# Kernel tuning notes

Hardware: AMD Instinct MI355X
Metric: run time of the kernel (lower is better)

## Reference

```python
import jax, jax.numpy as jnp
import numpy as np

B, S, D = 4, 2048, 1024
LAYERS = 2
NLOPS = 4
GAMMA = 0.01          # lindblad_gamma
COND_TH = 100.0       # condition_threshold
EPS = 1e-6


def setup_inputs() -> dict:
    key = jax.random.key(0)
    ks = jax.random.split(key, 9)
    x_real = jax.random.normal(ks[0], (B, S, D), jnp.float32)
    x_imag = jax.random.normal(ks[1], (B, S, D), jnp.float32)
    H_prev = jax.random.uniform(ks[2], (B, D, D), jnp.float32)
    eye = jnp.eye(D, dtype=jnp.float32)
    # base mixing layer (stand-in for ComplexMamba3Layer): near-identity complex linear
    W_real = eye[None, :, :] + 0.02 * jax.random.normal(ks[3], (LAYERS, D, D), jnp.float32)
    W_imag = 0.02 * jax.random.normal(ks[4], (LAYERS, D, D), jnp.float32)
    L_ops = 0.5 * jax.random.normal(ks[5], (LAYERS, NLOPS, D), jnp.float32)
    theta = jax.random.uniform(ks[6], (LAYERS,), jnp.float32, 0.0, 0.5)
    jump_scale = 0.9 * jnp.ones((LAYERS,), jnp.float32)
    kappa_th = 0.1 * jnp.ones((LAYERS,), jnp.float32)   # curvature_threshold per layer
    return dict(x_real=x_real, x_imag=x_imag, H_prev=H_prev,
                W_real=W_real, W_imag=W_imag, L_ops=L_ops,
                theta=theta, jump_scale=jump_scale, kappa_th=kappa_th)


def _v8_forward(x_real, x_imag, H_prev, W_real, W_imag, L_ops, theta, jump_scale, kappa_th):
    psi = jax.lax.complex(x_real, x_imag)  # [B,S,D] complex64
    Hp = H_prev                            # [B,D,D] real (prev Hamiltonian, detached)
    for l in range(LAYERS):
        residual = psi
        # --- base layer: complex linear mix ---
        Wc = jax.lax.complex(W_real[l], W_imag[l])
        out = jnp.einsum('bsd,de->bse', psi, Wc)
        branch_delta = out - residual
        # --- delta-RMS normalize (no_grad -> stop_gradient) ---
        rms = jnp.sqrt(jnp.clip(jnp.mean(branch_delta.real ** 2 + branch_delta.imag ** 2), 1e-12, None))
        rms = jax.lax.stop_gradient(jnp.maximum(rms, 1e-3))
        b = branch_delta / rms
        # --- Lindblad dissipation: diagonal damping gamma * sum_k L_k^2 ---
        damp = GAMMA * jnp.sum(L_ops[l] ** 2, axis=0)  # [D]
        b = b * (1.0 - damp)
        # --- approximate Hamiltonian H = (1/S) sum_s |psi_s><psi_s| (no_grad) ---
        mag = jnp.abs(b)                                # [B,S,D]
        H = jax.lax.stop_gradient(jnp.einsum('bsd,bse->bde', mag, mag) / S)  # [B,D,D]
        # --- hybrid automata: curvature K = ||H - Hp||_F / ||Hp||_F ---
        diff_n = jnp.sqrt(jnp.sum((H - Hp) ** 2, axis=(1, 2)))
        prev_n = jnp.sqrt(jnp.sum(Hp ** 2, axis=(1, 2)))
        K = diff_n / (prev_n + EPS)                     # [B]
        jumped = K > kappa_th[l]
        b = jnp.where(jumped[:, None, None], b * jump_scale[l].astype(jnp.complex64), b)
        Hp = H
        # --- quaternionic escape: diag-based condition estimate, phase rotation ---
        dg = jnp.diagonal(H, axis1=1, axis2=2)          # [B,D]
        cond = jnp.max(dg, axis=1) / (jnp.min(dg, axis=1) + 1e-12)
        escaped = cond > COND_TH
        rot = jnp.exp(1j * theta[l]).astype(jnp.complex64)
        b = jnp.where(escaped[:, None, None], b * rot, b)
        # --- rescale and residual ---
        b = b * rms
        psi = residual + b
    return jnp.stack([psi.real, psi.imag], axis=0)  # [2,B,S,D] float32


def reference(x_real, x_imag, H_prev, W_real, W_imag, L_ops, theta, jump_scale, kappa_th):
    return _v8_forward(x_real, x_imag, H_prev, W_real, W_imag, L_ops, theta, jump_scale, kappa_th)
```

## Files before the change

kernel.cpp:

```cpp
#include <hip/hip_runtime.h>

#define B_ 4
#define S_ 2048
#define D_ 1024
#define M_ (B_*S_)
#define K2_ 2048
#define N2_ 2048
#define NTOT (B_*S_*D_)
#define DD (D_*D_)

typedef __attribute__((ext_vector_type(4))) float f32x4;
typedef __attribute__((ext_vector_type(8))) short short8;
typedef __attribute__((ext_vector_type(4))) unsigned short u16x4;
typedef __attribute__((ext_vector_type(8))) unsigned short u16x8;

static __device__ __forceinline__ unsigned short f2bf(float f) {
    union { float f; unsigned int u; } v; v.f = f;
    unsigned int u = v.u;
    unsigned int r = (u + 0x7fffu + ((u >> 16) & 1u)) >> 16;
    return (unsigned short)r;
}
static __device__ __forceinline__ float bf2f(unsigned short h) {
    union { unsigned int u; float f; } v; v.u = ((unsigned int)h) << 16;
    return v.f;
}


__global__ __launch_bounds__(256, 2) void gemm_main2(const unsigned short* __restrict__ A2,
                                                     const unsigned short* __restrict__ B2T,
                                                     unsigned short* __restrict__ bd2,
                                                     unsigned short* __restrict__ magT,
                                                     float* __restrict__ scal, int l)
{
    __shared__ unsigned short smem[3 * 128 * 64];
    __shared__ float red[4];
    unsigned short* As  = smem;
    unsigned short* Bsr = smem + 8192;
    unsigned short* Bsi = smem + 16384;

    f32x4 accr[4][4], acci[4][4];
#pragma unroll
    for (int i = 0; i < 4; ++i)
#pragma unroll
        for (int j = 0; j < 4; ++j) { accr[i][j] = (f32x4)0.0f; acci[i][j] = (f32x4)0.0f; }

    const int nt = blockIdx.x, mt = blockIdx.y;
    const int tid = threadIdx.x, wave = tid >> 6, lane = tid & 63;
    const int q = lane >> 4, lm = lane & 15;
    const int wm = (wave >> 1) * 64, wn = (wave & 1) * 64;
    const int crow = lane >> 3;
    const int gcol = ((lane & 7) ^ crow) * 8;

    const unsigned short* Ag  = A2  + (long)mt * 128 * K2_;
    const unsigned short* Bgr = B2T + (long)(nt * 128) * K2_;
    const unsigned short* Bgi = B2T + (long)(nt * 128 + 1024) * K2_;

    for (int kt = 0; kt < K2_ / 64; ++kt) {
        const long k0 = (long)kt * 64;
        __syncthreads();
#pragma unroll
        for (int i2 = 0; i2 < 4; ++i2) {
            int c   = i2 * 4 + wave;
            int row = c * 8 + crow;
            long go = (long)row * K2_ + k0 + gcol;
            __builtin_amdgcn_global_load_lds((const __attribute__((address_space(1))) void*)(Ag + go),
                                             (__attribute__((address_space(3))) void*)(As + c * 512), 16, 0, 0);
            __builtin_amdgcn_global_load_lds((const __attribute__((address_space(1))) void*)(Bgr + go),
                                             (__attribute__((address_space(3))) void*)(Bsr + c * 512), 16, 0, 0);
            __builtin_amdgcn_global_load_lds((const __attribute__((address_space(1))) void*)(Bgi + go),
                                             (__attribute__((address_space(3))) void*)(Bsi + c * 512), 16, 0, 0);
        }
        __syncthreads();
#pragma unroll
        for (int kk = 0; kk < 64; kk += 32) {
            short8 a[4], br[4], bi[4];
#pragma unroll
            for (int t = 0; t < 4; ++t) {
                int arow  = wm + t * 16 + lm;
                int aslot = ((kk >> 3) + q) ^ (arow & 7);
                a[t] = *(const short8*)(As + arow * 64 + aslot * 8);
                int brow  = wn + t * 16 + lm;
                int bslot = ((kk >> 3) + q) ^ (brow & 7);
                br[t] = *(const short8*)(Bsr + brow * 64 + bslot * 8);
                bi[t] = *(const short8*)(Bsi + brow * 64 + bslot * 8);
            }
#pragma unroll
            for (int um = 0; um < 4; ++um)
#pragma unroll
                for (int un = 0; un < 4; ++un) {
                    accr[um][un] = __builtin_amdgcn_mfma_f32_16x16x32_bf16(a[um], br[un], accr[um][un], 0, 0, 0);
                    acci[um][un] = __builtin_amdgcn_mfma_f32_16x16x32_bf16(a[um], bi[un], acci[um][un], 0, 0, 0);
                }
        }
    }

    __syncthreads();
    unsigned short* magLds = smem;
    float ss = 0.f;
#pragma unroll
    for (int um = 0; um < 4; ++um) {
#pragma unroll
        for (int un = 0; un < 4; ++un) {
            int colb = wn + un * 16 + lm;
            int coln = nt * 128 + colb;
            u16x4 magv;
#pragma unroll
            for (int i = 0; i < 4; ++i) {
                long rowm = (long)mt * 128 + wm + um * 16 + q * 4 + i;
                float vr = accr[um][un][i];
                float vi = acci[um][un][i];
                bd2[rowm * N2_ + coln]        = f2bf(vr);
                bd2[rowm * N2_ + 1024 + coln] = f2bf(vi);
                float s2 = vr * vr + vi * vi;
                ss += s2;
                magv[i] = f2bf(sqrtf(s2));
            }
            *(u16x4*)(magLds + colb * 136 + wm + um * 16 + q * 4) = magv;
        }
    }
    for (int off = 32; off > 0; off >>= 1) ss += __shfl_down(ss, off);
    if (lane == 0) red[wave] = ss;
    __syncthreads();
    if (tid == 0) atomicAdd(scal + l, red[0] + red[1] + red[2] + red[3]);

    const int b   = mt >> 4;
    const long s0 = (long)(mt & 15) * 128;
#pragma unroll
    for (int it = 0; it < 8; ++it) {
        int sid = it * 256 + tid;
        int row = sid >> 4, seg = sid & 15;
        unsigned short* dst = magT + (long)b * D_ * S_ + (long)(nt * 128 + row) * S_ + s0 + seg * 8;
        *(u16x8*)dst = *(const u16x8*)(magLds + row * 136 + seg * 8);
    }
}

__device__ __forceinline__ void mfma_gemm_128(const unsigned short* __restrict__ Ag, long astride,
                                              const unsigned short* __restrict__ Bg, long bstride,
                                              int kiters,
                                              unsigned short* As, unsigned short* Bs,
                                              f32x4 acc[4][4])
{
    const int tid  = threadIdx.x;
    const int wave = tid >> 6, lane = tid & 63;
    const int q    = lane >> 4, lm = lane & 15;
    const int wm   = (wave >> 1) * 64, wn = (wave & 1) * 64;
    const int crow = lane >> 3;
    const int gcol = ((lane & 7) ^ crow) * 8;

    for (int kt = 0; kt < kiters; ++kt) {
        const long k0 = (long)kt * 64;
        __syncthreads();
#pragma unroll
        for (int i2 = 0; i2 < 4; ++i2) {
            int c   = i2 * 4 + wave;
            int row = c * 8 + crow;
            const unsigned short* ga = Ag + (long)row * astride + k0 + gcol;
            const unsigned short* gb = Bg + (long)row * bstride + k0 + gcol;
            __builtin_amdgcn_global_load_lds((const __attribute__((address_space(1))) void*)ga,
                                             (__attribute__((address_space(3))) void*)(As + c * 512), 16, 0, 0);
            __builtin_amdgcn_global_load_lds((const __attribute__((address_space(1))) void*)gb,
                                             (__attribute__((address_space(3))) void*)(Bs + c * 512), 16, 0, 0);
        }
        __syncthreads();
#pragma unroll
        for (int kk = 0; kk < 64; kk += 32) {
            short8 a[4], b[4];
#pragma unroll
            for (int t = 0; t < 4; ++t) {
                int arow  = wm + t * 16 + lm;
                int aslot = ((kk >> 3) + q) ^ (arow & 7);
                a[t] = *(const short8*)(As + arow * 64 + aslot * 8);
                int brow  = wn + t * 16 + lm;
                int bslot = ((kk >> 3) + q) ^ (brow & 7);
                b[t] = *(const short8*)(Bs + brow * 64 + bslot * 8);
            }
#pragma unroll
            for (int um = 0; um < 4; ++um)
#pragma unroll
                for (int un = 0; un < 4; ++un)
                    acc[um][un] = __builtin_amdgcn_mfma_f32_16x16x32_bf16(a[um], b[un], acc[um][un], 0, 0, 0);
        }
    }
}

__global__ __launch_bounds__(256, 2) void gemmH_split(const unsigned short* __restrict__ magT,
                                                      float* __restrict__ pbuf)
{
    __shared__ unsigned short As[128 * 64];
    __shared__ unsigned short Bs[128 * 64];
    f32x4 acc[4][4];
#pragma unroll
    for (int i = 0; i < 4; ++i)
#pragma unroll
        for (int j = 0; j < 4; ++j) acc[i][j] = (f32x4)0.0f;

    const int pair = blockIdx.x, b = blockIdx.y, kc = blockIdx.z;
    int idx = pair, ty = 0;
    while (idx >= 8 - ty) { idx -= 8 - ty; ++ty; }
    const int tx = ty + idx;

    const unsigned short* Mb = magT + (long)b * D_ * S_ + (long)kc * 512;
    mfma_gemm_128(Mb + (long)ty * 128 * S_, S_,
                  Mb + (long)tx * 128 * S_, S_, 8, As, Bs, acc);

    float* pt = pbuf + ((long)(kc * 36 + pair) * B_ + b) * 16384;
    const int tid = threadIdx.x, wave = tid >> 6, lane = tid & 63;
    const int q = lane >> 4, lm = lane & 15;
    const int wm = (wave >> 1) * 64, wn = (wave & 1) * 64;
#pragma unroll
    for (int um = 0; um < 4; ++um)
#pragma unroll
        for (int un = 0; un < 4; ++un) {
            int c = wn + un * 16 + lm;
#pragma unroll
            for (int i = 0; i < 4; ++i) {
                int r = wm + um * 16 + q * 4 + i;
                pt[r * 128 + c] = acc[um][un][i];
            }
        }
}

__global__ __launch_bounds__(256) void reduce_H(const float* __restrict__ pbuf,
                                                const float* __restrict__ Hp,
                                                float* __restrict__ H,
                                                float* __restrict__ scal,
                                                const float* __restrict__ dampv, int l)
{
    __shared__ float redd[4], redp[4];
    const int pair = blockIdx.x, b = blockIdx.y;
    int idx0 = pair, ty = 0;
    while (idx0 >= 8 - ty) { idx0 -= 8 - ty; ++ty; }
    const int tx = ty + idx0;
    const int diag_tile = (tx == ty);

    float mean = fmaxf(scal[l] / (float)NTOT, 1e-12f);
    float inv  = 1.0f / fmaxf(sqrtf(mean), 1e-3f);
    const float scale = inv * inv / (float)S_;

    const int tid = threadIdx.x;
    float d2 = 0.f, p2 = 0.f;
    float dmx = 0.f, dmn = 3.402823466e38f;
    for (int it = 0; it < 64; ++it) {
        int idx = it * 256 + tid;
        int r = idx >> 7, c = idx & 127;
        int gr = ty * 128 + r, gc = tx * 128 + c;
        float s = pbuf[((long)(0 * 36 + pair) * B_ + b) * 16384 + idx]
                + pbuf[((long)(1 * 36 + pair) * B_ + b) * 16384 + idx]
                + pbuf[((long)(2 * 36 + pair) * B_ + b) * 16384 + idx]
                + pbuf[((long)(3 * 36 + pair) * B_ + b) * 16384 + idx];
        float h = s * scale * dampv[gr] * dampv[gc];
        long adr = (long)b * DD + (long)gr * D_ + gc;
        if (l == 0) {
            float hp1 = Hp[adr];
            H[adr] = h;
            float df1 = h - hp1;
            if (diag_tile) {
                d2 += df1 * df1; p2 += hp1 * hp1;
            } else {
                float hp2 = Hp[(long)b * DD + (long)gc * D_ + gr];
                float df2 = h - hp2;
                d2 += df1 * df1 + df2 * df2;
                p2 += hp1 * hp1 + hp2 * hp2;
            }
        } else {
            float hp1 = Hp[adr];
            float df1 = h - hp1;
            float w = diag_tile ? 1.0f : 2.0f;
            d2 += w * df1 * df1;
            p2 += w * hp1 * hp1;
        }
        if (diag_tile && gr == gc) { dmx = fmaxf(dmx, h); dmn = fminf(dmn, h); }
    }
    int lane = tid & 63, wave = tid >> 6;
    for (int off = 32; off > 0; off >>= 1) { d2 += __shfl_down(d2, off); p2 += __shfl_down(p2, off); }
    if (lane == 0) { redd[wave] = d2; redp[wave] = p2; }
    if (diag_tile) {
        atomicMax((int*)scal + 18 + l * 4 + b, __float_as_int(dmx));
        atomicMin((int*)scal + 26 + l * 4 + b, __float_as_int(dmn));
    }
    __syncthreads();
    if (tid == 0) {
        atomicAdd(scal + 2 + l * 4 + b,  redd[0] + redd[1] + redd[2] + redd[3]);
        atomicAdd(scal + 10 + l * 4 + b, redp[0] + redp[1] + redp[2] + redp[3]);
    }
}

__global__ void init_kernel(const float* __restrict__ xr, const float* __restrict__ xi,
                            unsigned short* __restrict__ A2, float* __restrict__ scal)
{
    if (blockIdx.x == 0 && threadIdx.x < 34)
        scal[threadIdx.x] = (threadIdx.x >= 26) ? 3.402823466e38f : 0.0f;
    long t = (long)blockIdx.x * 256 + threadIdx.x;
    long i = t * 4;
    f32x4 r  = *(const f32x4*)(xr + i);
    f32x4 im = *(const f32x4*)(xi + i);
    long m = i / D_; int d = (int)(i % D_);
    u16x4 rr, ii;
#pragma unroll
    for (int j = 0; j < 4; ++j) { rr[j] = f2bf(r[j]); ii[j] = f2bf(im[j]); }
    *(u16x4*)(A2 + m * K2_ + d) = rr;
    *(u16x4*)(A2 + m * K2_ + D_ + d) = ii;
}

__global__ __launch_bounds__(256) void pack_b2t(const float* __restrict__ Wr_all,
                                                const float* __restrict__ Wi_all,
                                                unsigned short* __restrict__ B2T, int l)
{
    __shared__ float T[64][65];
    const float* Wr = Wr_all + (long)l * DD;
    const float* Wi = Wi_all + (long)l * DD;
    int k0 = blockIdx.x * 64;
    int n0 = blockIdx.y * 64;
    int t = threadIdx.x;
#pragma unroll
    for (int it = 0; it < 16; ++it) {
        int idx = it * 256 + t;
        int kl = idx >> 6, nl = idx & 63;
        int k = k0 + kl, n = n0 + nl;
        float v;
        if (k < D_) v = (n < D_) ? Wr[k * D_ + n] : Wi[k * D_ + (n - D_)];
        else        v = (n < D_) ? -Wi[(k - D_) * D_ + n] : Wr[(k - D_) * D_ + (n - D_)];
        if (k == n) v -= 1.0f;
        T[kl][nl] = v;
    }
    __syncthreads();
#pragma unroll
    for (int it = 0; it < 16; ++it) {
        int idx = it * 256 + t;
        int nl = idx >> 6, kl = idx & 63;
        B2T[(long)(n0 + nl) * K2_ + (k0 + kl)] = f2bf(T[kl][nl]);
    }
}

__global__ void damp_kernel(const float* __restrict__ Lops, float* __restrict__ dampv)
{
    int g = blockIdx.x;
    int l = g >> 2;
    int d = (g & 3) * 256 + threadIdx.x;
    const float* Lp = Lops + (long)l * 4 * D_;
    float s = 0.f;
#pragma unroll
    for (int k = 0; k < 4; ++k) { float v = Lp[k * D_ + d]; s += v * v; }
    dampv[l * D_ + d] = 1.0f - 0.01f * s;
}

__global__ void update_kernel(const unsigned short* __restrict__ bd2,
                              const float* __restrict__ dampv,
                              const float* __restrict__ scal,
                              const float* __restrict__ theta,
                              const float* __restrict__ jscale,
                              const float* __restrict__ kappa, int l,
                              const float* __restrict__ src_r,
                              const float* __restrict__ src_i,
                              float* __restrict__ dst_r,
                              float* __restrict__ dst_i,
                              unsigned short* __restrict__ A2,
                              int write_a2)
{
    long t = (long)blockIdx.x * 256 + threadIdx.x;
    long i = t * 4;
    long m = i / D_; int d = (int)(i % D_);
    int b = (int)(m >> 11);

    float dn = sqrtf(scal[2 + l * 4 + b]);
    float pn = sqrtf(scal[10 + l * 4 + b]);
    float K  = dn / (pn + 1e-6f);
    float mx = __int_as_float(((const int*)scal)[18 + l * 4 + b]);
    float mn = __int_as_float(((const int*)scal)[26 + l * 4 + b]);
    int jumped  = K > kappa[l];
    int escaped = (mx / (mn + 1e-12f)) > 100.0f;
    float js = jumped ? jscale[l] : 1.0f;
    float th = theta[l];
    float fr = js * (escaped ? cosf(th) : 1.0f);
    float fi = js * (escaped ? sinf(th) : 0.0f);

    u16x4 brv = *(const u16x4*)(bd2 + m * N2_ + d);
    u16x4 biv = *(const u16x4*)(bd2 + m * N2_ + D_ + d);
    f32x4 w  = *(const f32x4*)(dampv + d);
    f32x4 pr = *(const f32x4*)(src_r + i);
    f32x4 pi = *(const f32x4*)(src_i + i);
    u16x4 ar, ai;
#pragma unroll
    for (int j = 0; j < 4; ++j) {
        float br = bf2f(brv[j]) * w[j];
        float bi = bf2f(biv[j]) * w[j];
        float nr = pr[j] + br * fr - bi * fi;
        float ni = pi[j] + br * fi + bi * fr;
        pr[j] = nr; pi[j] = ni;
        ar[j] = f2bf(nr); ai[j] = f2bf(ni);
    }
    *(f32x4*)(dst_r + i) = pr;
    *(f32x4*)(dst_i + i) = pi;
    if (write_a2) {
        *(u16x4*)(A2 + m * K2_ + d) = ar;
        *(u16x4*)(A2 + m * K2_ + D_ + d) = ai;
    }
}

extern "C" void kernel_launch(void* const* d_in, const int* in_sizes, int n_in,
                              void* d_out, int out_size, void* d_ws, size_t ws_size,
                              hipStream_t stream)
{
    const float* xr     = (const float*)d_in[0];
    const float* xi     = (const float*)d_in[1];
    const float* Hprev  = (const float*)d_in[2];
    const float* Wr     = (const float*)d_in[3];
    const float* Wi     = (const float*)d_in[4];
    const float* Lops   = (const float*)d_in[5];
    const float* theta  = (const float*)d_in[6];
    const float* jscale = (const float*)d_in[7];
    const float* kappa  = (const float*)d_in[8];

    float* psi_r = (float*)d_out;
    float* psi_i = psi_r + NTOT;

    char* ws = (char*)d_ws;
    unsigned short* A2   = (unsigned short*)ws;
    float* pbuf          = (float*)ws;
    unsigned short* B2T  = (unsigned short*)(ws + 33554432);
    unsigned short* bd2  = (unsigned short*)(ws + 41943040);
    unsigned short* magT = (unsigned short*)(ws + 75497472);
    float* H             = (float*)(ws + 92274688);
    float* scal          = (float*)(ws + 109051904);
    float* dampv         = scal + 64;

    init_kernel<<<NTOT / 4 / 256, 256, 0, stream>>>(xr, xi, A2, scal);
    damp_kernel<<<8, 256, 0, stream>>>(Lops, dampv);

    for (int l = 0; l < 2; ++l) {
        pack_b2t<<<dim3(32, 32), 256, 0, stream>>>(Wr, Wi, B2T, l);
        gemm_main2<<<dim3(8, M_ / 128), 256, 0, stream>>>(A2, B2T, bd2, magT, scal, l);
        gemmH_split<<<dim3(36, B_, 4), 256, 0, stream>>>(magT, pbuf);
        reduce_H<<<dim3(36, B_), 256, 0, stream>>>(
            pbuf, (l == 0) ? Hprev : H, H, scal, dampv + l * D_, l);
        update_kernel<<<NTOT / 4 / 256, 256, 0, stream>>>(
            bd2, dampv + l * D_, scal, theta, jscale, kappa, l,
            (l == 0) ? xr : psi_r, (l == 0) ? xi : psi_i,
            psi_r, psi_i, A2, l == 0);
    }
}
```

Measured before the change: 487.5 us.

## Accumulate split-K Gram tiles atomically and keep compact layer-0 Gram for comparison

The H Gram GEMM now atomically adds its four split-K partials into one zeroed packed-tile buffer, replacing a separate 4-way partial buffer that the reduce pass had to read. The finalize pass no longer writes the full dense H matrix. For layer 1 it rebuilds the previous H on the fly from the packed layer-0 Gram tiles using the layer-0 scale and damping. This cuts reduction traffic and the dense H write, at the cost of float atomics (nondeterministic summation order), two extra memsets, and a higher occupancy hint on the GEMM.

```diff
diff --git a/kernel.cpp b/kernel.cpp
--- a/kernel.cpp
+++ b/kernel.cpp
@@ -8,6 +8,8 @@
 #define N2_ 2048
 #define NTOT (B_*S_*D_)
 #define DD (D_*D_)
+#define NPAIR 36
+#define GBYTES (B_*NPAIR*16384*4)
 
 typedef __attribute__((ext_vector_type(4))) float f32x4;
 typedef __attribute__((ext_vector_type(8))) short short8;
@@ -183,8 +185,8 @@
     }
 }
 
-__global__ __launch_bounds__(256, 2) void gemmH_split(const unsigned short* __restrict__ magT,
-                                                      float* __restrict__ pbuf)
+__global__ __launch_bounds__(256, 4) void gemm_H(const unsigned short* __restrict__ magT,
+                                                 float* __restrict__ G)
 {
     __shared__ unsigned short As[128 * 64];
     __shared__ unsigned short Bs[128 * 64];
@@ -203,7 +205,7 @@
     mfma_gemm_128(Mb + (long)ty * 128 * S_, S_,
                   Mb + (long)tx * 128 * S_, S_, 8, As, Bs, acc);
 
-    float* pt = pbuf + ((long)(kc * 36 + pair) * B_ + b) * 16384;
+    float* gt = G + ((long)b * NPAIR + pair) * 16384;
     const int tid = threadIdx.x, wave = tid >> 6, lane = tid & 63;
     const int q = lane >> 4, lm = lane & 15;
     const int wm = (wave >> 1) * 64, wn = (wave & 1) * 64;
@@ -215,16 +217,16 @@
 #pragma unroll
             for (int i = 0; i < 4; ++i) {
                 int r = wm + um * 16 + q * 4 + i;
-                pt[r * 128 + c] = acc[um][un][i];
+                atomicAdd(gt + r * 128 + c, acc[um][un][i]);
             }
         }
 }
 
-__global__ __launch_bounds__(256) void reduce_H(const float* __restrict__ pbuf,
-                                                const float* __restrict__ Hp,
-                                                float* __restrict__ H,
-                                                float* __restrict__ scal,
-                                                const float* __restrict__ dampv, int l)
+__global__ __launch_bounds__(256) void finalize_H(const float* __restrict__ G,
+                                                  const float* __restrict__ G0,
+                                                  const float* __restrict__ Hprev,
+                                                  float* __restrict__ scal,
+                                                  const float* __restrict__ dampv, int l)
 {
     __shared__ float redd[4], redp[4];
     const int pair = blockIdx.x, b = blockIdx.y;
@@ -236,6 +238,17 @@
     float mean = fmaxf(scal[l] / (float)NTOT, 1e-12f);
     float inv  = 1.0f / fmaxf(sqrtf(mean), 1e-3f);
     const float scale = inv * inv / (float)S_;
+    float scale0 = 0.f;
+    if (l == 1) {
+        float mean0 = fmaxf(scal[0] / (float)NTOT, 1e-12f);
+        float inv0  = 1.0f / fmaxf(sqrtf(mean0), 1e-3f);
+        scale0 = inv0 * inv0 / (float)S_;
+    }
+    const float* dl = dampv + (long)l * D_;
+    const float* d0 = dampv;
+
+    const float* gt  = G  + ((long)b * NPAIR + pair) * 16384;
+    const float* gt0 = (l == 1) ? (G0 + ((long)b * NPAIR + pair) * 16384) : nullptr;
 
     const int tid = threadIdx.x;
     float d2 = 0.f, p2 = 0.f;
@@ -244,30 +257,24 @@
         int idx = it * 256 + tid;
         int r = idx >> 7, c = idx & 127;
         int gr = ty * 128 + r, gc = tx * 128 + c;
-        float s = pbuf[((long)(0 * 36 + pair) * B_ + b) * 16384 + idx]
-                + pbuf[((long)(1 * 36 + pair) * B_ + b) * 16384 + idx]
-                + pbuf[((long)(2 * 36 + pair) * B_ + b) * 16384 + idx]
-                + pbuf[((long)(3 * 36 + pair) * B_ + b) * 16384 + idx];
-        float h = s * scale * dampv[gr] * dampv[gc];
-        long adr = (long)b * DD + (long)gr * D_ + gc;
+        float h = gt[idx] * scale * dl[gr] * dl[gc];
         if (l == 0) {
-            float hp1 = Hp[adr];
-            H[adr] = h;
+            float hp1 = Hprev[(long)b * DD + (long)gr * D_ + gc];
             float df1 = h - hp1;
             if (diag_tile) {
                 d2 += df1 * df1; p2 += hp1 * hp1;
             } else {
-                float hp2 = Hp[(long)b * DD + (long)gc * D_ + gr];
+                float hp2 = Hprev[(long)b * DD + (long)gc * D_ + gr];
                 float df2 = h - hp2;
                 d2 += df1 * df1 + df2 * df2;
                 p2 += hp1 * hp1 + hp2 * hp2;
             }
         } else {
-            float hp1 = Hp[adr];
-            float df1 = h - hp1;
+            float hp = gt0[idx] * scale0 * d0[gr] * d0[gc];
+            float df = h - hp;
             float w = diag_tile ? 1.0f : 2.0f;
-            d2 += w * df1 * df1;
-            p2 += w * hp1 * hp1;
+            d2 += w * df * df;
+            p2 += w * hp * hp;
         }
         if (diag_tile && gr == gc) { dmx = fmaxf(dmx, h); dmn = fminf(dmn, h); }
     }
@@ -416,26 +423,32 @@
 
     char* ws = (char*)d_ws;
     unsigned short* A2   = (unsigned short*)ws;
-    float* pbuf          = (float*)ws;
+    float* G1            = (float*)ws;
     unsigned short* B2T  = (unsigned short*)(ws + 33554432);
     unsigned short* bd2  = (unsigned short*)(ws + 41943040);
     unsigned short* magT = (unsigned short*)(ws + 75497472);
-    float* H             = (float*)(ws + 92274688);
+    float* G0            = (float*)(ws + 92274688);
     float* scal          = (float*)(ws + 109051904);
     float* dampv         = scal + 64;
 
     init_kernel<<<NTOT / 4 / 256, 256, 0, stream>>>(xr, xi, A2, scal);
     damp_kernel<<<8, 256, 0, stream>>>(Lops, dampv);
-
-    for (int l = 0; l < 2; ++l) {
-        pack_b2t<<<dim3(32, 32), 256, 0, stream>>>(Wr, Wi, B2T, l);
-        gemm_main2<<<dim3(8, M_ / 128), 256, 0, stream>>>(A2, B2T, bd2, magT, scal, l);
-        gemmH_split<<<dim3(36, B_, 4), 256, 0, stream>>>(magT, pbuf);
-        reduce_H<<<dim3(36, B_), 256, 0, stream>>>(
-            pbuf, (l == 0) ? Hprev : H, H, scal, dampv + l * D_, l);
-        update_kernel<<<NTOT / 4 / 256, 256, 0, stream>>>(
-            bd2, dampv + l * D_, scal, theta, jscale, kappa, l,
-            (l == 0) ? xr : psi_r, (l == 0) ? xi : psi_i,
-            psi_r, psi_i, A2, l == 0);
-    }
-}
+    (void)hipMemsetAsync(G0, 0, GBYTES, stream);
+
+    pack_b2t<<<dim3(32, 32), 256, 0, stream>>>(Wr, Wi, B2T, 0);
+    gemm_main2<<<dim3(8, M_ / 128), 256, 0, stream>>>(A2, B2T, bd2, magT, scal, 0);
+    gemm_H<<<dim3(NPAIR, B_, 4), 256, 0, stream>>>(magT, G0);
+    finalize_H<<<dim3(NPAIR, B_), 256, 0, stream>>>(G0, nullptr, Hprev, scal, dampv, 0);
+    update_kernel<<<NTOT / 4 / 256, 256, 0, stream>>>(
+        bd2, dampv, scal, theta, jscale, kappa, 0,
+        xr, xi, psi_r, psi_i, A2, 1);
+
+    pack_b2t<<<dim3(32, 32), 256, 0, stream>>>(Wr, Wi, B2T, 1);
+    gemm_main2<<<dim3(8, M_ / 128), 256, 0, stream>>>(A2, B2T, bd2, magT, scal, 1);
+    (void)hipMemsetAsync(G1, 0, GBYTES, stream);
+    gemm_H<<<dim3(NPAIR, B_, 4), 256, 0, stream>>>(magT, G1);
+    finalize_H<<<dim3(NPAIR, B_), 256, 0, stream>>>(G1, G0, nullptr, scal, dampv, 1);
+    update_kernel<<<NTOT / 4 / 256, 256, 0, stream>>>(
+        bd2, dampv + D_, scal, theta, jscale, kappa, 1,
+        psi_r, psi_i, psi_r, psi_i, (unsigned short*)nullptr, 0);
+}
```

Result: slower. 547.9 us (+12.4%).
